# Performance work log

Measured on AMD Instinct MI355X. Metric: run time of the kernel, lower is better.

## Reference

```python
import jax, jax.numpy as jnp
import numpy as np

B, H, W, DIM = 8, 56, 56, 512
WS, SS, HEADS = 7, 3, 16
HD = DIM // HEADS
NW_TOK = WS * WS  # 49 tokens per window


def _make_mask():
    # static additive attention mask for shifted windows (numpy, concrete)
    img = np.zeros((H, W), dtype=np.float32)
    slices = [slice(0, -WS), slice(-WS, -SS), slice(-SS, None)]
    cnt = 0
    for hs in slices:
        for ws_ in slices:
            img[hs, ws_] = cnt
            cnt += 1
    m = img.reshape(H // WS, WS, W // WS, WS).transpose(0, 2, 1, 3).reshape(-1, NW_TOK)
    diff = m[:, None, :] - m[:, :, None]
    return np.where(diff != 0, -np.inf, 0.0).astype(np.float32)  # (nW, 49, 49)

_MASK = jnp.asarray(_make_mask())


def _ln(x, w, b, eps=1e-5):
    mu = jnp.mean(x, axis=-1, keepdims=True)
    var = jnp.mean(jnp.square(x - mu), axis=-1, keepdims=True)
    return (x - mu) * jax.lax.rsqrt(var + eps) * w + b


def setup_inputs() -> dict:
    key = jax.random.key(0)
    ks = jax.random.split(key, 5)
    s = lambda fan: 1.0 / np.sqrt(fan)
    return {
        "x": jax.random.normal(ks[0], (B, H * W, DIM), jnp.float32),
        "ln1_w": jnp.ones((DIM,), jnp.float32),
        "ln1_b": jnp.zeros((DIM,), jnp.float32),
        "qkv_w": jax.random.normal(ks[1], (DIM, 3 * DIM), jnp.float32) * s(DIM),
        "qkv_b": jnp.zeros((3 * DIM,), jnp.float32),
        "proj_w": jax.random.normal(ks[2], (DIM, DIM), jnp.float32) * s(DIM),
        "proj_b": jnp.zeros((DIM,), jnp.float32),
        "ln2_w": jnp.ones((DIM,), jnp.float32),
        "ln2_b": jnp.zeros((DIM,), jnp.float32),
        "fc1_w": jax.random.normal(ks[3], (DIM, 2 * DIM), jnp.float32) * s(DIM),
        "fc1_b": jnp.zeros((2 * DIM,), jnp.float32),
        "fc2_w": jax.random.normal(ks[4], (2 * DIM, DIM), jnp.float32) * s(2 * DIM),
        "fc2_b": jnp.zeros((DIM,), jnp.float32),
    }


def reference(x, ln1_w, ln1_b, qkv_w, qkv_b, proj_w, proj_b, ln2_w, ln2_b, fc1_w, fc1_b, fc2_w, fc2_b):
    Bn = x.shape[0]
    xr = x.reshape(Bn, H, W, DIM)
    h = xr
    y = _ln(xr, ln1_w, ln1_b)
    y = jnp.roll(y, shift=(-SS, -SS), axis=(1, 2))
    # window partition: (Bn*nW, 49, DIM)
    win = y.reshape(Bn, H // WS, WS, W // WS, WS, DIM).transpose(0, 1, 3, 2, 4, 5)
    win = win.reshape(-1, NW_TOK, DIM)
    nWtot = win.shape[0]
    # window attention
    qkv = (win @ qkv_w + qkv_b).reshape(nWtot, NW_TOK, 3, HEADS, HD)
    q, k, v = (qkv[:, :, i].transpose(0, 2, 1, 3) for i in range(3))  # (nWtot, heads, 49, hd)
    attn = jnp.einsum('whqd,whkd->whqk', q * (HD ** -0.5), k)
    nW = _MASK.shape[0]
    attn = attn.reshape(Bn, nW, HEADS, NW_TOK, NW_TOK) + _MASK[None, :, None]
    attn = jax.nn.softmax(attn, axis=-1).reshape(nWtot, HEADS, NW_TOK, NW_TOK)
    out = jnp.einsum('whqk,whkd->whqd', attn, v)
    out = out.transpose(0, 2, 1, 3).reshape(nWtot, NW_TOK, DIM)
    out = out @ proj_w + proj_b
    # window reverse
    out = out.reshape(Bn, H // WS, W // WS, WS, WS, DIM).transpose(0, 1, 3, 2, 4, 5)
    out = out.reshape(Bn, H, W, DIM)
    out = jnp.roll(out, shift=(SS, SS), axis=(1, 2))
    x2 = (h + out).reshape(Bn, H * W, DIM)
    # MLP block
    z = _ln(x2, ln2_w, ln2_b)
    z = jax.nn.gelu(z @ fc1_w + fc1_b) @ fc2_w + fc2_b
    return x2 + z
```

## Files before the change

kernel.cpp:

```cpp
#include <hip/hip_runtime.h>

typedef unsigned short u16;
typedef unsigned short u16x8 __attribute__((ext_vector_type(8)));
typedef __bf16         bf16x8 __attribute__((ext_vector_type(8)));
typedef float          f32x4  __attribute__((ext_vector_type(4)));

#define DIM 512
#define LTOK 25088

__device__ __forceinline__ float bf2f(u16 u) {
  union { unsigned int i; float f; } c; c.i = ((unsigned int)u) << 16; return c.f;
}
__device__ __forceinline__ u16 f2bf(float f) {
  union { float f; unsigned int i; } c; c.f = f;
  unsigned int i = c.i;
  return (u16)((i + 0x7FFFu + ((i >> 16) & 1u)) >> 16);
}
__device__ __forceinline__ float gelu_tanh(float x) {
  float x2 = x * x;
  float y2 = x * (1.5957691216057308f + 0.0713548162726f * x2);
  return x / (1.0f + __expf(-y2));
}
__device__ __forceinline__ void gload16(const u16* g, u16* l) {
  __builtin_amdgcn_global_load_lds(
      (__attribute__((address_space(1))) void*)(u16*)g,
      (__attribute__((address_space(3))) void*)l,
      16, 0, 0);
}
__device__ __forceinline__ int rowToToken(int row) {
  int win = row / 49, t = row - win * 49;
  int b = win >> 6, wi = win & 63;
  int hr = (wi >> 3) * 7 + t / 7;
  int wr = (wi & 7) * 7 + t % 7;
  int hs = hr + 3; if (hs >= 56) hs -= 56;
  int ws2 = wr + 3; if (ws2 >= 56) ws2 -= 56;
  return b * 3136 + hs * 56 + ws2;
}

__global__ __launch_bounds__(256) void ln1_kernel(const float* __restrict__ x,
    const float* __restrict__ w, const float* __restrict__ b, u16* __restrict__ out) {
  int r = blockIdx.x * 4 + (threadIdx.x >> 6);
  int lane = threadIdx.x & 63;
  int tok = rowToToken(r);
  const float* src = x + (size_t)tok * DIM + lane * 8;
  float v[8]; float s = 0.f, ss = 0.f;
  f32x4 v0 = *(const f32x4*)(src);
  f32x4 v1 = *(const f32x4*)(src + 4);
  #pragma unroll
  for (int j = 0; j < 4; ++j) { v[j] = v0[j]; v[j + 4] = v1[j]; }
  #pragma unroll
  for (int j = 0; j < 8; ++j) { s += v[j]; ss += v[j] * v[j]; }
  #pragma unroll
  for (int off = 32; off > 0; off >>= 1) { s += __shfl_xor(s, off); ss += __shfl_xor(ss, off); }
  float mean = s * (1.0f / 512.0f);
  float var  = ss * (1.0f / 512.0f) - mean * mean;
  float rstd = rsqrtf(var + 1e-5f);
  f32x4 w0 = *(const f32x4*)(w + lane * 8), w1 = *(const f32x4*)(w + lane * 8 + 4);
  f32x4 b0 = *(const f32x4*)(b + lane * 8), b1 = *(const f32x4*)(b + lane * 8 + 4);
  u16x8 o;
  #pragma unroll
  for (int j = 0; j < 4; ++j) {
    o[j]     = f2bf((v[j]     - mean) * rstd * w0[j] + b0[j]);
    o[j + 4] = f2bf((v[j + 4] - mean) * rstd * w1[j] + b1[j]);
  }
  *(u16x8*)(out + (size_t)r * DIM + lane * 8) = o;
}

__global__ __launch_bounds__(256) void ln2_kernel(const float* __restrict__ x2,
    const float* __restrict__ w, const float* __restrict__ b, u16* __restrict__ out) {
  int r = blockIdx.x * 4 + (threadIdx.x >> 6);
  int lane = threadIdx.x & 63;
  const float* src = x2 + (size_t)r * DIM + lane * 8;
  float v[8]; float s = 0.f, ss = 0.f;
  f32x4 v0 = *(const f32x4*)(src);
  f32x4 v1 = *(const f32x4*)(src + 4);
  #pragma unroll
  for (int j = 0; j < 4; ++j) { v[j] = v0[j]; v[j + 4] = v1[j]; }
  #pragma unroll
  for (int j = 0; j < 8; ++j) { s += v[j]; ss += v[j] * v[j]; }
  #pragma unroll
  for (int off = 32; off > 0; off >>= 1) { s += __shfl_xor(s, off); ss += __shfl_xor(ss, off); }
  float mean = s * (1.0f / 512.0f);
  float var  = ss * (1.0f / 512.0f) - mean * mean;
  float rstd = rsqrtf(var + 1e-5f);
  f32x4 w0 = *(const f32x4*)(w + lane * 8), w1 = *(const f32x4*)(w + lane * 8 + 4);
  f32x4 b0 = *(const f32x4*)(b + lane * 8), b1 = *(const f32x4*)(b + lane * 8 + 4);
  u16x8 o;
  #pragma unroll
  for (int j = 0; j < 4; ++j) {
    o[j]     = f2bf((v[j]     - mean) * rstd * w0[j] + b0[j]);
    o[j + 4] = f2bf((v[j + 4] - mean) * rstd * w1[j] + b1[j]);
  }
  *(u16x8*)(out + (size_t)r * DIM + lane * 8) = o;
}

__global__ __launch_bounds__(256) void transpose_kernel(const float* __restrict__ in,
    u16* __restrict__ out, int K, int N) {
  __shared__ u16 tile[32][33];
  int tx = threadIdx.x & 31, ty = threadIdx.x >> 5;
  int n0 = blockIdx.x * 32, k0 = blockIdx.y * 32;
  #pragma unroll
  for (int r = 0; r < 4; ++r) {
    int kr = ty + r * 8;
    tile[kr][tx] = f2bf(in[(size_t)(k0 + kr) * N + n0 + tx]);
  }
  __syncthreads();
  #pragma unroll
  for (int r = 0; r < 4; ++r) {
    int nr = ty + r * 8;
    out[(size_t)(n0 + nr) * K + k0 + tx] = tile[tx][nr];
  }
}

template<int MODE, int N, int KD>
__global__ __launch_bounds__(256) void gemm_kernel(
    const u16* __restrict__ A, const u16* __restrict__ Bt,
    const float* __restrict__ bias, void* outp,
    const float* resF) {
  __shared__ __align__(16) u16 lA[2][8192];
  __shared__ __align__(16) u16 lB[2][8192];
  int tid = threadIdx.x;
  int lane = tid & 63, wid = tid >> 6;
  int wm = wid >> 1, wn = wid & 1;
  int m0 = blockIdx.x * 128, n0 = blockIdx.y * 128;
  int l15 = lane & 15, l4 = lane >> 4;
  f32x4 acc[4][4];
  #pragma unroll
  for (int i = 0; i < 4; ++i)
    #pragma unroll
    for (int j = 0; j < 4; ++j) acc[i][j] = (f32x4){0.f, 0.f, 0.f, 0.f};

  auto stage = [&](int buf, int k0) {
    #pragma unroll
    for (int is = 0; is < 4; ++is) {
      int e = is * 2048 + tid * 8;
      int mm = e >> 6;
      int kk = (e & 63) ^ ((mm & 7) << 3);
      gload16(A  + (size_t)(m0 + mm) * KD + k0 + kk, &lA[buf][is * 2048 + wid * 512]);
      gload16(Bt + (size_t)(n0 + mm) * KD + k0 + kk, &lB[buf][is * 2048 + wid * 512]);
    }
  };
  auto compute = [&](int buf) {
    #pragma unroll
    for (int ks = 0; ks < 2; ++ks) {
      bf16x8 af[4], bfv[4];
      int ksw = (ks * 32 + l4 * 8) ^ ((l15 & 7) << 3);
      #pragma unroll
      for (int i = 0; i < 4; ++i)
        af[i] = *(const bf16x8*)&lA[buf][(wm * 64 + i * 16 + l15) * 64 + ksw];
      #pragma unroll
      for (int j = 0; j < 4; ++j)
        bfv[j] = *(const bf16x8*)&lB[buf][(wn * 64 + j * 16 + l15) * 64 + ksw];
      __builtin_amdgcn_s_setprio(1);
      #pragma unroll
      for (int i = 0; i < 4; ++i)
        #pragma unroll
        for (int j = 0; j < 4; ++j)
          acc[i][j] = __builtin_amdgcn_mfma_f32_16x16x32_bf16(af[i], bfv[j], acc[i][j], 0, 0, 0);
      __builtin_amdgcn_s_setprio(0);
    }
  };

  stage(0, 0);
  __syncthreads();
  int cur = 0;
  for (int t = 0; t < KD / 64 - 1; ++t) {
    stage(cur ^ 1, (t + 1) * 64);
    compute(cur);
    __syncthreads();
    cur ^= 1;
  }
  compute(cur);

  #pragma unroll
  for (int i = 0; i < 4; ++i) {
    #pragma unroll
    for (int j = 0; j < 4; ++j) {
      int col = n0 + wn * 64 + j * 16 + l15;
      float bcol = bias[col];
      #pragma unroll
      for (int r = 0; r < 4; ++r) {
        int row = m0 + wm * 64 + i * 16 + l4 * 4 + r;
        float v = acc[i][j][r] + bcol;
        if constexpr (MODE == 0) {
          ((u16*)outp)[(size_t)row * N + col] = f2bf(v);
        } else if constexpr (MODE == 1) {
          int tok = rowToToken(row);
          size_t idx = (size_t)tok * DIM + col;
          ((float*)outp)[idx] = v + resF[idx];
        } else if constexpr (MODE == 2) {
          ((u16*)outp)[(size_t)row * N + col] = f2bf(gelu_tanh(v));
        } else {
          size_t idx = (size_t)row * N + col;
          ((float*)outp)[idx] = v + resF[idx];
        }
      }
    }
  }
}

__global__ __launch_bounds__(256) void attn_kernel(const u16* __restrict__ qkv,
                                                   u16* __restrict__ out) {
  int win = blockIdx.x;
  int wi = win & 63;
  int tid = threadIdx.x, lane = tid & 63, wid = tid >> 6;
  int l15 = lane & 15, l4 = lane >> 4;
  __shared__ int codes[49];
  __shared__ __align__(16) u16 plds[4][64 * 72];
  if (tid < 49) {
    int hr = (wi >> 3) * 7 + tid / 7;
    int wr = (wi & 7) * 7 + tid % 7;
    int rh = (hr < 49) ? 0 : (hr < 53 ? 1 : 2);
    int rw = (wr < 49) ? 0 : (wr < 53 ? 1 : 2);
    codes[tid] = rh * 3 + rw;
  }
  __syncthreads();
  int ck[4], cq[4][4];
  #pragma unroll
  for (int j = 0; j < 4; ++j) {
    int c = 16 * j + l15;
    ck[j] = (c < 49) ? codes[c] : -1;
  }
  #pragma unroll
  for (int i = 0; i < 4; ++i)
    #pragma unroll
    for (int r = 0; r < 4; ++r) {
      int row = 16 * i + 4 * l4 + r;
      cq[i][r] = codes[row < 49 ? row : 48];
    }
  size_t wbase = (size_t)win * 49 * 1536;
  u16* pw = plds[wid];
  const float scale = 0.17677669529663687f;

  for (int hh = 0; hh < 4; ++hh) {
    int head = wid * 4 + hh;
    size_t hoff = wbase + (size_t)head * 32;

    bf16x8 vf[2][2];
    #pragma unroll
    for (int ks = 0; ks < 2; ++ks)
      #pragma unroll
      for (int jn = 0; jn < 2; ++jn) {
        u16x8 tmp;
        #pragma unroll
        for (int j = 0; j < 8; ++j) {
          int tok = ks * 32 + l4 * 8 + j; tok = tok < 49 ? tok : 48;
          tmp[j] = qkv[hoff + (size_t)tok * 1536 + 1024 + jn * 16 + l15];
        }
        vf[ks][jn] = __builtin_bit_cast(bf16x8, tmp);
      }

    bf16x8 qf[4], kf[4];
    #pragma unroll
    for (int i = 0; i < 4; ++i) {
      int tr = 16 * i + l15; tr = tr < 49 ? tr : 48;
      qf[i] = *(const bf16x8*)(qkv + hoff + (size_t)tr * 1536 + l4 * 8);
      kf[i] = *(const bf16x8*)(qkv + hoff + (size_t)tr * 1536 + 512 + l4 * 8);
    }

    f32x4 acc[4][4];
    #pragma unroll
    for (int i = 0; i < 4; ++i)
      #pragma unroll
      for (int j = 0; j < 4; ++j) acc[i][j] = (f32x4){0.f, 0.f, 0.f, 0.f};
    #pragma unroll
    for (int i = 0; i < 4; ++i)
      #pragma unroll
      for (int j = 0; j < 4; ++j)
        acc[i][j] = __builtin_amdgcn_mfma_f32_16x16x32_bf16(qf[i], kf[j], acc[i][j], 0, 0, 0);

    #pragma unroll
    for (int i = 0; i < 4; ++i) {
      #pragma unroll
      for (int r = 0; r < 4; ++r) {
        float s0[4];
        float m = -1e30f;
        #pragma unroll
        for (int j = 0; j < 4; ++j) {
          float s_ = acc[i][j][r] * scale;
          s_ = (ck[j] == cq[i][r]) ? s_ : -1e30f;
          s0[j] = s_;
          m = fmaxf(m, s_);
        }
        m = fmaxf(m, __shfl_xor(m, 1));
        m = fmaxf(m, __shfl_xor(m, 2));
        m = fmaxf(m, __shfl_xor(m, 4));
        m = fmaxf(m, __shfl_xor(m, 8));
        float sum = 0.f;
        #pragma unroll
        for (int j = 0; j < 4; ++j) { s0[j] = __expf(s0[j] - m); sum += s0[j]; }
        sum += __shfl_xor(sum, 1);
        sum += __shfl_xor(sum, 2);
        sum += __shfl_xor(sum, 4);
        sum += __shfl_xor(sum, 8);
        float inv = 1.0f / sum;
        int row = 16 * i + 4 * l4 + r;
        #pragma unroll
        for (int j = 0; j < 4; ++j)
          pw[row * 72 + 16 * j + l15] = f2bf(s0[j] * inv);
      }
    }

    f32x4 oacc[4][2];
    #pragma unroll
    for (int i = 0; i < 4; ++i)
      #pragma unroll
      for (int jn = 0; jn < 2; ++jn) oacc[i][jn] = (f32x4){0.f, 0.f, 0.f, 0.f};
    #pragma unroll
    for (int ks = 0; ks < 2; ++ks) {
      bf16x8 pf[4];
      #pragma unroll
      for (int i = 0; i < 4; ++i)
        pf[i] = *(const bf16x8*)&pw[(16 * i + l15) * 72 + ks * 32 + l4 * 8];
      #pragma unroll
      for (int i = 0; i < 4; ++i)
        #pragma unroll
        for (int jn = 0; jn < 2; ++jn)
          oacc[i][jn] = __builtin_amdgcn_mfma_f32_16x16x32_bf16(pf[i], vf[ks][jn], oacc[i][jn], 0, 0, 0);
    }

    #pragma unroll
    for (int i = 0; i < 4; ++i) {
      int row = 16 * i + 4 * l4;
      #pragma unroll
      for (int jn = 0; jn < 2; ++jn)
        #pragma unroll
        for (int r = 0; r < 4; ++r)
          if (row + r < 49)
            out[((size_t)win * 49 + row + r) * 512 + head * 32 + jn * 16 + l15] =
                f2bf(oacc[i][jn][r]);
    }
  }
}

extern "C" void kernel_launch(void* const* d_in, const int* in_sizes, int n_in,
                              void* d_out, int out_size, void* d_ws, size_t ws_size,
                              hipStream_t stream) {
  const float* x     = (const float*)d_in[0];
  const float* ln1w  = (const float*)d_in[1];
  const float* ln1b  = (const float*)d_in[2];
  const float* qkvw  = (const float*)d_in[3];
  const float* qkvb  = (const float*)d_in[4];
  const float* projw = (const float*)d_in[5];
  const float* projb = (const float*)d_in[6];
  const float* ln2w  = (const float*)d_in[7];
  const float* ln2b  = (const float*)d_in[8];
  const float* fc1w  = (const float*)d_in[9];
  const float* fc1b  = (const float*)d_in[10];
  const float* fc2w  = (const float*)d_in[11];
  const float* fc2b  = (const float*)d_in[12];
  float* outF = (float*)d_out;

  u16* wsu     = (u16*)d_ws;
  u16* qkv_wt  = wsu;
  u16* proj_wt = qkv_wt  + 512 * 1536;
  u16* fc1_wt  = proj_wt + 512 * 512;
  u16* fc2_wt  = fc1_wt  + 512 * 1024;
  u16* xw      = fc2_wt  + 1024 * 512;
  u16* qkvB    = xw + (size_t)LTOK * 512;
  u16* attnO   = xw;
  u16* z_in    = xw;
  u16* z1      = qkvB;
  float* x2    = outF;

  transpose_kernel<<<dim3(1536 / 32, 512 / 32), 256, 0, stream>>>(qkvw, qkv_wt, 512, 1536);
  transpose_kernel<<<dim3(512 / 32, 512 / 32),  256, 0, stream>>>(projw, proj_wt, 512, 512);
  transpose_kernel<<<dim3(1024 / 32, 512 / 32), 256, 0, stream>>>(fc1w, fc1_wt, 512, 1024);
  transpose_kernel<<<dim3(512 / 32, 1024 / 32), 256, 0, stream>>>(fc2w, fc2_wt, 1024, 512);

  ln1_kernel<<<LTOK / 4, 256, 0, stream>>>(x, ln1w, ln1b, xw);

  gemm_kernel<0, 1536, 512><<<dim3(196, 12), 256, 0, stream>>>(xw, qkv_wt, qkvb, qkvB, nullptr);

  attn_kernel<<<512, 256, 0, stream>>>(qkvB, attnO);

  gemm_kernel<1, 512, 512><<<dim3(196, 4), 256, 0, stream>>>(attnO, proj_wt, projb, x2, x);

  ln2_kernel<<<LTOK / 4, 256, 0, stream>>>(x2, ln2w, ln2b, z_in);

  gemm_kernel<2, 1024, 512><<<dim3(196, 8), 256, 0, stream>>>(z_in, fc1_wt, fc1b, z1, nullptr);

  gemm_kernel<3, 512, 1024><<<dim3(196, 4), 256, 0, stream>>>(z1, fc2_wt, fc2b, outF, x2);
}
```

Baseline: 420.5 us.

## Load GEMM B operand directly from global into registers instead of LDS

The weight (B) tile is no longer staged through shared memory. Each wave now loads its B fragments straight from global memory into registers, double-buffered across K steps, and the main loop is unrolled by two so the register buffers stay static. This halves LDS use and removes the LDS reads for B, which could raise occupancy. In exchange it uses many more vector registers, makes each wave fetch its own copy of B (the two wm waves load the same data), and adds global-load latency directly in front of the MFMAs.

```diff
diff --git a/kernel.cpp b/kernel.cpp
--- a/kernel.cpp
+++ b/kernel.cpp
@@ -118,7 +118,6 @@
     const float* __restrict__ bias, void* outp,
     const float* resF) {
   __shared__ __align__(16) u16 lA[2][8192];
-  __shared__ __align__(16) u16 lB[2][8192];
   int tid = threadIdx.x;
   int lane = tid & 63, wid = tid >> 6;
   int wm = wid >> 1, wn = wid & 1;
@@ -130,47 +129,56 @@
     #pragma unroll
     for (int j = 0; j < 4; ++j) acc[i][j] = (f32x4){0.f, 0.f, 0.f, 0.f};
 
-  auto stage = [&](int buf, int k0) {
+  auto stageA = [&](int buf, int k0) {
     #pragma unroll
     for (int is = 0; is < 4; ++is) {
       int e = is * 2048 + tid * 8;
       int mm = e >> 6;
       int kk = (e & 63) ^ ((mm & 7) << 3);
-      gload16(A  + (size_t)(m0 + mm) * KD + k0 + kk, &lA[buf][is * 2048 + wid * 512]);
-      gload16(Bt + (size_t)(n0 + mm) * KD + k0 + kk, &lB[buf][is * 2048 + wid * 512]);
+      gload16(A + (size_t)(m0 + mm) * KD + k0 + kk, &lA[buf][is * 2048 + wid * 512]);
     }
   };
-  auto compute = [&](int buf) {
+  auto loadB = [&](int k0, bf16x8 (&bv)[2][4]) {
+    #pragma unroll
+    for (int ks = 0; ks < 2; ++ks)
+      #pragma unroll
+      for (int j = 0; j < 4; ++j)
+        bv[ks][j] = *(const bf16x8*)(Bt + (size_t)(n0 + wn * 64 + j * 16 + l15) * KD
+                                        + k0 + ks * 32 + l4 * 8);
+  };
+  auto compute = [&](int buf, bf16x8 (&bv)[2][4]) {
     #pragma unroll
     for (int ks = 0; ks < 2; ++ks) {
-      bf16x8 af[4], bfv[4];
+      bf16x8 af[4];
       int ksw = (ks * 32 + l4 * 8) ^ ((l15 & 7) << 3);
       #pragma unroll
       for (int i = 0; i < 4; ++i)
         af[i] = *(const bf16x8*)&lA[buf][(wm * 64 + i * 16 + l15) * 64 + ksw];
-      #pragma unroll
-      for (int j = 0; j < 4; ++j)
-        bfv[j] = *(const bf16x8*)&lB[buf][(wn * 64 + j * 16 + l15) * 64 + ksw];
       __builtin_amdgcn_s_setprio(1);
       #pragma unroll
       for (int i = 0; i < 4; ++i)
         #pragma unroll
         for (int j = 0; j < 4; ++j)
-          acc[i][j] = __builtin_amdgcn_mfma_f32_16x16x32_bf16(af[i], bfv[j], acc[i][j], 0, 0, 0);
+          acc[i][j] = __builtin_amdgcn_mfma_f32_16x16x32_bf16(af[i], bv[ks][j], acc[i][j], 0, 0, 0);
       __builtin_amdgcn_s_setprio(0);
     }
   };
 
-  stage(0, 0);
+  bf16x8 b0[2][4], b1[2][4];
+  constexpr int NK = KD / 64;
+  stageA(0, 0);
+  loadB(0, b0);
   __syncthreads();
-  int cur = 0;
-  for (int t = 0; t < KD / 64 - 1; ++t) {
-    stage(cur ^ 1, (t + 1) * 64);
-    compute(cur);
+  #pragma unroll
+  for (int t = 0; t < NK; t += 2) {
+    if (t + 1 < NK) { stageA(1, (t + 1) * 64); loadB((t + 1) * 64, b1); }
+    compute(0, b0);
     __syncthreads();
-    cur ^= 1;
-  }
-  compute(cur);
+    if (t + 1 >= NK) break;
+    if (t + 2 < NK) { stageA(0, (t + 2) * 64); loadB((t + 2) * 64, b0); }
+    compute(1, b1);
+    __syncthreads();
+  }
 
   #pragma unroll
   for (int i = 0; i < 4; ++i) {
```

Result: slower. 548.9 us (+30.6%).
